# Kernel optimization log

Measured on AMD Instinct MI355X. Metric: run time of the kernel, lower is better.

Reference implementation:

```python
import jax, jax.numpy as jnp
import numpy as np

B, N, NFEAT, NHID, NHEADS, NCLASS, K1 = 4, 2048, 256, 64, 4, 32, 256
ALPHA = 0.2      # leaky relu slope
NEG = -9e15      # mask value used by the torch impl


def setup_inputs() -> dict:
    key = jax.random.key(0)
    ks = jax.random.split(key, 16)
    s = 0.05
    return {
        "x": jax.random.normal(ks[0], (B, N, NFEAT), jnp.float32),
        "adj": jax.random.randint(ks[1], (B, N, N), 0, 2).astype(jnp.int32),
        "one_hop_idcs": jax.random.randint(ks[2], (B, K1), 0, N),
        # multi-head GAT layer params (stacked over heads)
        "W": jax.random.normal(ks[3], (NHEADS, NFEAT, NHID), jnp.float32) * s,
        "a1": jax.random.normal(ks[4], (NHEADS, NHID), jnp.float32) * s,  # a[:nhid]
        "a2": jax.random.normal(ks[5], (NHEADS, NHID), jnp.float32) * s,  # a[nhid:]
        # output GAT layer params
        "Wo": jax.random.normal(ks[6], (NHEADS * NHID, NCLASS), jnp.float32) * s,
        "ao1": jax.random.normal(ks[7], (NCLASS,), jnp.float32) * s,
        "ao2": jax.random.normal(ks[8], (NCLASS,), jnp.float32) * s,
        # classifier: Linear(32, nclass) -> PReLU(nclass) -> Linear(nclass, 2)
        "W1": jax.random.normal(ks[9], (NCLASS, NCLASS), jnp.float32) * s,
        "b1": jnp.zeros((NCLASS,), jnp.float32),
        "prelu_w": jnp.full((NCLASS,), 0.25, jnp.float32),
        "W2": jax.random.normal(ks[10], (NCLASS, 2), jnp.float32) * s,
        "b2": jnp.zeros((2,), jnp.float32),
    }


def _gat_heads(x, W, a1, a2, adj):
    """Dense multi-head GAT. e_ij = leakyrelu(a^T [Wh_i || Wh_j]) computed
    as broadcast of two rank-1 projections (no [N,N,2d] concat tensor)."""
    Wh = jnp.einsum('bnf,hfd->bhnd', x, W)                 # [B,H,N,d]
    f1 = jnp.einsum('bhnd,hd->bhn', Wh, a1)                # src term
    f2 = jnp.einsum('bhnd,hd->bhn', Wh, a2)                # dst term
    e = jax.nn.leaky_relu(f1[:, :, :, None] + f2[:, :, None, :], ALPHA)
    e = jnp.where(adj[:, None, :, :] > 0, e, NEG)
    attn = jax.nn.softmax(e, axis=-1)                      # [B,H,N,N]
    h = jnp.einsum('bhnm,bhmd->bhnd', attn, Wh)            # [B,H,N,d]
    h = jax.nn.elu(h)                                      # concat=True -> elu
    # concat heads: [B,N,H*d]
    return h.transpose(0, 2, 1, 3).reshape(x.shape[0], x.shape[1], -1)


def _gat_out(x, Wo, ao1, ao2, adj):
    Wh = x @ Wo                                            # [B,N,nclass]
    f1 = Wh @ ao1
    f2 = Wh @ ao2
    e = jax.nn.leaky_relu(f1[:, :, None] + f2[:, None, :], ALPHA)
    e = jnp.where(adj > 0, e, NEG)
    attn = jax.nn.softmax(e, axis=-1)
    return attn @ Wh                                       # concat=False -> no elu here


def reference(x, adj, one_hop_idcs, W, a1, a2, Wo, ao1, ao2,
              W1, b1, prelu_w, W2, b2):
    h = _gat_heads(x, W, a1, a2, adj)          # [B,N,H*nhid]
    h = jax.nn.elu(_gat_out(h, Wo, ao1, ao2, adj))  # [B,N,nclass]
    # vectorized per-batch gather (replaces python loop over b)
    ef = jnp.take_along_axis(h, one_hop_idcs[:, :, None], axis=1)  # [B,K1,nclass]
    ef = ef.reshape(-1, h.shape[-1])
    y = ef @ W1 + b1
    y = jnp.where(y > 0, y, prelu_w * y)       # PReLU(nclass)
    return y @ W2 + b2                         # [B*K1, 2]
```

## Files before the change

kernel.cpp:

```cpp
#include <hip/hip_runtime.h>
#include <hip/hip_bf16.h>
#include <stdint.h>
#include <math.h>

#define BB 4
#define NN 2048
#define NFEAT 256
#define NHID 64
#define NHEADS 4
#define NCLASS 32
#define KK1 256
#define ALPHA 0.2f
#define LOG2E 1.4426950408889634f

typedef _Float16 f16x8 __attribute__((ext_vector_type(8)));
typedef _Float16 f16x4 __attribute__((ext_vector_type(4)));
typedef _Float16 h16x2 __attribute__((ext_vector_type(2)));
typedef float f32x4 __attribute__((ext_vector_type(4)));

__device__ __forceinline__ f16x8 ld8(const _Float16* p){
  f16x8 r;
  *(f16x4*)&r = *(const f16x4*)p;
  *((f16x4*)&r + 1) = *(const f16x4*)(p + 4);
  return r;
}

__device__ __forceinline__ h16x2 pk2(float a, float b){
  auto v = __builtin_amdgcn_cvt_pkrtz(a, b);
  h16x2 r;
  __builtin_memcpy(&r, &v, sizeof(r));
  return r;
}

__global__ void __launch_bounds__(256) pack_adj(const int* __restrict__ adj,
                                                unsigned long long* __restrict__ bits,
                                                int* __restrict__ cnt){
  __shared__ int csum[4];
  int row = blockIdx.x;
  const int* arow = adj + (size_t)row * NN;
  int lane = threadIdx.x & 63, wv = threadIdx.x >> 6;
  int c = 0;
  #pragma unroll
  for (int it=0; it<NN/256; ++it){
    int j = it*256 + threadIdx.x;
    unsigned long long m = __ballot(arow[j] > 0);
    if (lane==0){ bits[(size_t)row*(NN/64) + it*4 + wv] = m; c += __popcll(m); }
  }
  if (lane==0) csum[wv] = c;
  __syncthreads();
  if (threadIdx.x==0) cnt[row] = csum[0]+csum[1]+csum[2]+csum[3];
}

__global__ void __launch_bounds__(256) wh_proj2(const float* __restrict__ x,
        const float* __restrict__ W, const float* __restrict__ a1, const float* __restrict__ a2,
        _Float16* __restrict__ whT, float* __restrict__ f1l, float* __restrict__ f2l){
  __shared__ __align__(16) float xs[64*65];
  __shared__ float red1[4][64];
  __shared__ float red2[4][64];
  int bh = blockIdx.x >> 5;
  int i0 = (blockIdx.x & 31) * 64;
  int b = bh >> 2, h = bh & 3;
  int tid = threadIdx.x;
  int lane = tid & 63;
  int dbase = __builtin_amdgcn_readfirstlane(tid >> 6) * 16;
  float acc[16];
  #pragma unroll
  for (int dd=0; dd<16; ++dd) acc[dd] = 0.f;
  for (int kc=0; kc<4; ++kc){
    int kb = kc*64;
    __syncthreads();
    #pragma unroll
    for (int t=0; t<4; ++t){
      int row = t*16 + (tid>>4);
      int f4 = (tid&15)*4;
      float4 v = *(const float4*)(x + ((size_t)(b*NN + i0 + row))*NFEAT + kb + f4);
      xs[row*65 + f4 + 0] = v.x;
      xs[row*65 + f4 + 1] = v.y;
      xs[row*65 + f4 + 2] = v.z;
      xs[row*65 + f4 + 3] = v.w;
    }
    __syncthreads();
    const float* Wb = W + (size_t)h*NFEAT*NHID + (size_t)kb*NHID + dbase;
    #pragma unroll 4
    for (int f=0; f<64; ++f){
      float xv = xs[lane*65 + f];
      const float* wr = Wb + f*NHID;
      #pragma unroll
      for (int dd=0; dd<16; ++dd) acc[dd] = fmaf(xv, wr[dd], acc[dd]);
    }
  }
  float p1 = 0.f, p2 = 0.f;
  #pragma unroll
  for (int dd=0; dd<16; ++dd){
    int d = dbase + dd;
    whT[((size_t)bh*NHID + d)*NN + i0 + lane] = (_Float16)acc[dd];
    p1 = fmaf(acc[dd], a1[h*NHID + d], p1);
    p2 = fmaf(acc[dd], a2[h*NHID + d], p2);
  }
  int wv = tid >> 6;
  red1[wv][lane] = p1;
  red2[wv][lane] = p2;
  __syncthreads();
  if (tid < 64){
    float s1 = red1[0][tid]+red1[1][tid]+red1[2][tid]+red1[3][tid];
    float s2 = red2[0][tid]+red2[1][tid]+red2[2][tid]+red2[3][tid];
    f1l[(size_t)bh*NN + i0 + tid] = s1 * LOG2E;
    f2l[(size_t)bh*NN + i0 + tid] = s2 * LOG2E;
  }
}

__global__ void __launch_bounds__(256) attn_l1(
        const unsigned long long* __restrict__ bits,
        const _Float16* __restrict__ whT,
        const float* __restrict__ f1l, const float* __restrict__ f2l,
        const int* __restrict__ cnt_in,
        float* __restrict__ dst){
  const int JC = 128, PITCH = 132;
  __shared__ __align__(16) _Float16 whs[64*PITCH];
  __shared__ __align__(16) _Float16 wts[32*PITCH];
  __shared__ float ils[32];
  int tile = blockIdx.x & 63;
  int bh = blockIdx.x >> 6;
  int b = bh >> 2, h = bh & 3;
  int i0 = tile*32;
  int tid = threadIdx.x;
  int lane = tid & 63, wv = tid >> 6;
  int q = lane >> 4, col = lane & 15;
  int r = tid >> 3, jg = (tid & 7) * 16;
  float f1r = f1l[(size_t)bh*NN + i0 + r];
  bool czr = (cnt_in[b*NN + i0 + r] == 0);
  const unsigned short* mrow = (const unsigned short*)(bits + ((size_t)(b*NN + i0 + r))*(NN/64));
  const float* f2p = f2l + (size_t)bh*NN;
  const _Float16* whg = whT + (size_t)bh*NHID*NN;
  float lacc = 0.f;
  f32x4 c0 = {0.f,0.f,0.f,0.f}, c1 = {0.f,0.f,0.f,0.f};
  for (int it=0; it<NN/JC; ++it){
    __syncthreads();
    #pragma unroll
    for (int dd=0; dd<4; ++dd){
      int d = (tid>>4) + dd*16;
      int j8 = (tid&15)*8;
      uint4 v = *(const uint4*)(whg + (size_t)d*NN + it*JC + j8);
      uint2* w2 = (uint2*)&whs[d*PITCH + j8];
      w2[0] = uint2{v.x, v.y};
      w2[1] = uint2{v.z, v.w};
    }
    {
      unsigned int m16 = mrow[it*8 + (tid&7)];
      const float* fp = f2p + it*JC + jg;
      float4 fa = *(const float4*)(fp);
      float4 fb = *(const float4*)(fp+4);
      float4 fc = *(const float4*)(fp+8);
      float4 fd = *(const float4*)(fp+12);
      float fv[16] = {fa.x,fa.y,fa.z,fa.w, fb.x,fb.y,fb.z,fb.w,
                      fc.x,fc.y,fc.z,fc.w, fd.x,fd.y,fd.z,fd.w};
      h16x2 wp[8];
      #pragma unroll
      for (int p=0; p<8; ++p){
        float s0 = f1r + fv[2*p];
        float s1 = f1r + fv[2*p+1];
        s0 = (m16 & (1u<<(2*p)))   ? s0 : -1e5f;
        s1 = (m16 & (1u<<(2*p+1))) ? s1 : -1e5f;
        float e0 = fmaxf(s0, ALPHA*s0);
        float e1 = fmaxf(s1, ALPHA*s1);
        float w0 = exp2f(e0);
        float w1 = exp2f(e1);
        lacc += w0 + w1;
        wp[p] = pk2(w0, w1);
      }
      if (__builtin_expect(czr, 0)){
        h16x2 one2 = {(_Float16)1.f, (_Float16)1.f};
        #pragma unroll
        for (int p=0; p<8; ++p) wp[p] = one2;
      }
      uint2* wdst = (uint2*)&wts[r*PITCH + jg];
      const uint2* wsrc = (const uint2*)&wp[0];
      wdst[0]=wsrc[0]; wdst[1]=wsrc[1]; wdst[2]=wsrc[2]; wdst[3]=wsrc[3];
    }
    __syncthreads();
    #pragma unroll
    for (int ks=0; ks<4; ++ks){
      int kb = ks*32 + q*8;
      f16x8 a0 = ld8(&wts[col*PITCH + kb]);
      f16x8 a1v = ld8(&wts[(16+col)*PITCH + kb]);
      f16x8 bv = ld8(&whs[(wv*16+col)*PITCH + kb]);
      c0 = __builtin_amdgcn_mfma_f32_16x16x32_f16(a0, bv, c0, 0, 0, 0);
      c1 = __builtin_amdgcn_mfma_f32_16x16x32_f16(a1v, bv, c1, 0, 0, 0);
    }
  }
  lacc += __shfl_xor(lacc, 1, 64);
  lacc += __shfl_xor(lacc, 2, 64);
  lacc += __shfl_xor(lacc, 4, 64);
  if ((tid & 7) == 0) ils[r] = czr ? (1.0f/(float)NN) : 1.0f/lacc;
  __syncthreads();
  int dloc = wv*16 + col;
  #pragma unroll
  for (int mt=0; mt<2; ++mt){
    #pragma unroll
    for (int reg=0; reg<4; ++reg){
      int ir = mt*16 + q*4 + reg;
      float v = (mt==0 ? c0[reg] : c1[reg]) * ils[ir];
      v = v > 0.f ? v : expm1f(v);
      dst[((size_t)(b*NN + i0 + ir))*(NHEADS*NHID) + h*NHID + dloc] = v;
    }
  }
}

__global__ void __launch_bounds__(256) out_proj2(const float* __restrict__ h1,
        const float* __restrict__ Wo, const float* __restrict__ ao1, const float* __restrict__ ao2,
        _Float16* __restrict__ whT2, float* __restrict__ f1ol, float* __restrict__ f2ol){
  __shared__ __align__(16) float xs[64*65];
  __shared__ float red1[4][64];
  __shared__ float red2[4][64];
  int b = blockIdx.x >> 5;
  int i0 = (blockIdx.x & 31) * 64;
  int tid = threadIdx.x;
  int lane = tid & 63;
  int dbase = __builtin_amdgcn_readfirstlane(tid >> 6) * 8;
  float acc[8];
  #pragma unroll
  for (int dd=0; dd<8; ++dd) acc[dd] = 0.f;
  for (int kc=0; kc<4; ++kc){
    int kb = kc*64;
    __syncthreads();
    #pragma unroll
    for (int t=0; t<4; ++t){
      int row = t*16 + (tid>>4);
      int f4 = (tid&15)*4;
      float4 v = *(const float4*)(h1 + ((size_t)(b*NN + i0 + row))*256 + kb + f4);
      xs[row*65 + f4 + 0] = v.x;
      xs[row*65 + f4 + 1] = v.y;
      xs[row*65 + f4 + 2] = v.z;
      xs[row*65 + f4 + 3] = v.w;
    }
    __syncthreads();
    #pragma unroll 4
    for (int f=0; f<64; ++f){
      float xv = xs[lane*65 + f];
      const float* wr = Wo + (size_t)(kb+f)*NCLASS + dbase;
      #pragma unroll
      for (int dd=0; dd<8; ++dd) acc[dd] = fmaf(xv, wr[dd], acc[dd]);
    }
  }
  float p1 = 0.f, p2 = 0.f;
  #pragma unroll
  for (int dd=0; dd<8; ++dd){
    int d = dbase + dd;
    whT2[((size_t)b*NCLASS + d)*NN + i0 + lane] = (_Float16)acc[dd];
    p1 = fmaf(acc[dd], ao1[d], p1);
    p2 = fmaf(acc[dd], ao2[d], p2);
  }
  int wv = tid >> 6;
  red1[wv][lane] = p1;
  red2[wv][lane] = p2;
  __syncthreads();
  if (tid < 64){
    float s1 = red1[0][tid]+red1[1][tid]+red1[2][tid]+red1[3][tid];
    float s2 = red2[0][tid]+red2[1][tid]+red2[2][tid]+red2[3][tid];
    f1ol[(size_t)b*NN + i0 + tid] = s1 * LOG2E;
    f2ol[(size_t)b*NN + i0 + tid] = s2 * LOG2E;
  }
}

__global__ void __launch_bounds__(256) attn_l2(
        const unsigned long long* __restrict__ bits,
        const _Float16* __restrict__ whT2,
        const float* __restrict__ f1ol, const float* __restrict__ f2ol,
        const int* __restrict__ cnt_in, const int* __restrict__ oh,
        float* __restrict__ pc, float* __restrict__ pl){
  const int JC = 128, PITCH = 132;
  __shared__ __align__(16) _Float16 whs[32*PITCH];
  __shared__ __align__(16) _Float16 wts[32*PITCH];
  int blk = blockIdx.x;
  int js = blk & 7, kt = (blk>>3) & 7, b = blk >> 6;
  int tid = threadIdx.x;
  int lane = tid & 63, wv = tid >> 6;
  int q = lane >> 4, col = lane & 15;
  int r = tid >> 3, jg = (tid & 7) * 16;
  int row_i = oh[b*KK1 + kt*32 + r];
  float f1r = f1ol[b*NN + row_i];
  bool czr = (cnt_in[b*NN + row_i] == 0);
  const unsigned short* mrow = (const unsigned short*)(bits + ((size_t)(b*NN + row_i))*(NN/64));
  const float* f2p = f2ol + (size_t)b*NN;
  const _Float16* whg = whT2 + (size_t)b*NCLASS*NN;
  float lacc = 0.f;
  f32x4 c0 = {0.f,0.f,0.f,0.f};
  int mt = wv & 1, nt = wv >> 1;
  for (int ii=0; ii<2; ++ii){
    int it = js*2 + ii;
    __syncthreads();
    #pragma unroll
    for (int dd=0; dd<2; ++dd){
      int d = (tid>>4) + dd*16;
      int j8 = (tid&15)*8;
      uint4 v = *(const uint4*)(whg + (size_t)d*NN + it*JC + j8);
      uint2* w2 = (uint2*)&whs[d*PITCH + j8];
      w2[0] = uint2{v.x, v.y};
      w2[1] = uint2{v.z, v.w};
    }
    {
      unsigned int m16 = mrow[it*8 + (tid&7)];
      const float* fp = f2p + it*JC + jg;
      float4 fa = *(const float4*)(fp);
      float4 fb = *(const float4*)(fp+4);
      float4 fc = *(const float4*)(fp+8);
      float4 fd = *(const float4*)(fp+12);
      float fv[16] = {fa.x,fa.y,fa.z,fa.w, fb.x,fb.y,fb.z,fb.w,
                      fc.x,fc.y,fc.z,fc.w, fd.x,fd.y,fd.z,fd.w};
      h16x2 wp[8];
      #pragma unroll
      for (int p=0; p<8; ++p){
        float s0 = f1r + fv[2*p];
        float s1 = f1r + fv[2*p+1];
        s0 = (m16 & (1u<<(2*p)))   ? s0 : -1e5f;
        s1 = (m16 & (1u<<(2*p+1))) ? s1 : -1e5f;
        float e0 = fmaxf(s0, ALPHA*s0);
        float e1 = fmaxf(s1, ALPHA*s1);
        float w0 = exp2f(e0);
        float w1 = exp2f(e1);
        lacc += w0 + w1;
        wp[p] = pk2(w0, w1);
      }
      if (__builtin_expect(czr, 0)){
        h16x2 one2 = {(_Float16)1.f, (_Float16)1.f};
        #pragma unroll
        for (int p=0; p<8; ++p) wp[p] = one2;
        lacc += 16.f;
      }
      uint2* wdst = (uint2*)&wts[r*PITCH + jg];
      const uint2* wsrc = (const uint2*)&wp[0];
      wdst[0]=wsrc[0]; wdst[1]=wsrc[1]; wdst[2]=wsrc[2]; wdst[3]=wsrc[3];
    }
    __syncthreads();
    #pragma unroll
    for (int ks=0; ks<4; ++ks){
      int kb = ks*32 + q*8;
      f16x8 a0 = ld8(&wts[(mt*16+col)*PITCH + kb]);
      f16x8 bv = ld8(&whs[(nt*16+col)*PITCH + kb]);
      c0 = __builtin_amdgcn_mfma_f32_16x16x32_f16(a0, bv, c0, 0, 0, 0);
    }
  }
  lacc += __shfl_xor(lacc, 1, 64);
  lacc += __shfl_xor(lacc, 2, 64);
  lacc += __shfl_xor(lacc, 4, 64);
  if ((tid & 7) == 0) pl[blk*32 + r] = lacc;
  int dloc = nt*16 + col;
  #pragma unroll
  for (int reg=0; reg<4; ++reg){
    int ir = mt*16 + q*4 + reg;
    pc[(size_t)blk*1024 + ir*32 + dloc] = c0[reg];
  }
}

__global__ void __launch_bounds__(256) classify2(const float* __restrict__ pc,
        const float* __restrict__ pl,
        const float* __restrict__ W1, const float* __restrict__ b1,
        const float* __restrict__ pw, const float* __restrict__ W2, const float* __restrict__ b2,
        float* __restrict__ out){
  __shared__ float efs[4][32];
  int wv = threadIdx.x >> 6;
  int lane = threadIdx.x & 63;
  int row = blockIdx.x*4 + wv;
  int b = row >> 8, k = row & 255;
  int kt = k >> 5, r = k & 31;
  int base = (b*8 + kt)*8;
  if (lane < 32){
    float s = 0.f, l = 0.f;
    #pragma unroll
    for (int js=0; js<8; ++js){
      s += pc[(size_t)(base+js)*1024 + r*32 + lane];
      l += pl[(base+js)*32 + r];
    }
    float v = s / l;
    v = v > 0.f ? v : expm1f(v);
    efs[wv][lane] = v;
  }
  __syncthreads();
  const float* ef = efs[wv];
  int c = lane & 31;
  float y = b1[c];
  #pragma unroll 8
  for (int kk=0; kk<32; ++kk) y += ef[kk] * W1[kk*32 + c];
  y = y > 0.f ? y : pw[c]*y;
  float o0 = y * W2[c*2+0];
  float o1 = y * W2[c*2+1];
  #pragma unroll
  for (int o=16;o>0;o>>=1){ o0 += __shfl_xor(o0,o,64); o1 += __shfl_xor(o1,o,64); }
  if (lane==0){ out[row*2+0] = o0 + b2[0]; out[row*2+1] = o1 + b2[1]; }
}

extern "C" void kernel_launch(void* const* d_in, const int* in_sizes, int n_in,
                              void* d_out, int out_size, void* d_ws, size_t ws_size,
                              hipStream_t stream) {
  const float* x    = (const float*)d_in[0];
  const int*   adj  = (const int*)  d_in[1];
  const int*   oh   = (const int*)  d_in[2];
  const float* W    = (const float*)d_in[3];
  const float* a1   = (const float*)d_in[4];
  const float* a2   = (const float*)d_in[5];
  const float* Wo   = (const float*)d_in[6];
  const float* ao1  = (const float*)d_in[7];
  const float* ao2  = (const float*)d_in[8];
  const float* W1   = (const float*)d_in[9];
  const float* b1   = (const float*)d_in[10];
  const float* pw   = (const float*)d_in[11];
  const float* W2   = (const float*)d_in[12];
  const float* b2   = (const float*)d_in[13];
  float* out = (float*)d_out;

  char* base = (char*)d_ws;
  size_t off = 0;
  auto alloc = [&](size_t bytes)->char*{
    char* p = base + off;
    off = (off + bytes + 255) & ~(size_t)255;
    return p;
  };
  unsigned long long* adjbits = (unsigned long long*)alloc((size_t)BB*NN*(NN/64)*8);
  int*   cnt1 = (int*)  alloc((size_t)BB*NN*4);
  _Float16* WhT  = (_Float16*)alloc((size_t)BB*NHEADS*NHID*NN*2);
  float* f1l  = (float*)alloc((size_t)BB*NHEADS*NN*4);
  float* f2l  = (float*)alloc((size_t)BB*NHEADS*NN*4);
  float* h1   = (float*)alloc((size_t)BB*NN*(NHEADS*NHID)*4);
  _Float16* WhT2 = (_Float16*)alloc((size_t)BB*NCLASS*NN*2);
  float* f1ol = (float*)alloc((size_t)BB*NN*4);
  float* f2ol = (float*)alloc((size_t)BB*NN*4);
  float* pc   = (float*)alloc((size_t)256*1024*4);
  float* pl   = (float*)alloc((size_t)256*32*4);

  pack_adj<<<BB*NN, 256, 0, stream>>>(adj, adjbits, cnt1);
  wh_proj2<<<BB*NHEADS*(NN/64), 256, 0, stream>>>(x, W, a1, a2, WhT, f1l, f2l);
  attn_l1<<<BB*NHEADS*(NN/32), 256, 0, stream>>>(adjbits, WhT, f1l, f2l, cnt1, h1);
  out_proj2<<<BB*(NN/64), 256, 0, stream>>>(h1, Wo, ao1, ao2, WhT2, f1ol, f2ol);
  attn_l2<<<BB*8*8, 256, 0, stream>>>(adjbits, WhT2, f1ol, f2ol, cnt1, oh, pc, pl);
  classify2<<<(BB*KK1)/4, 256, 0, stream>>>(pc, pl, W1, b1, pw, W2, b2, out);
}
```

Baseline: 233.8 us.

## Double-buffer attn_l1 LDS tiles with register prefetch and branchless masking

```diff
diff --git a/kernel.cpp b/kernel.cpp
--- a/kernel.cpp
+++ b/kernel.cpp
@@ -30,6 +30,14 @@
   h16x2 r;
   __builtin_memcpy(&r, &v, sizeof(r));
   return r;
+}
+
+__device__ __forceinline__ float fexp2(float x){
+#if __has_builtin(__builtin_amdgcn_exp2f)
+  return __builtin_amdgcn_exp2f(x);
+#else
+  return exp2f(x);
+#endif
 }
 
 __global__ void __launch_bounds__(256) pack_adj(const int* __restrict__ adj,
@@ -115,9 +123,9 @@
         const float* __restrict__ f1l, const float* __restrict__ f2l,
         const int* __restrict__ cnt_in,
         float* __restrict__ dst){
-  const int JC = 128, PITCH = 132;
-  __shared__ __align__(16) _Float16 whs[64*PITCH];
-  __shared__ __align__(16) _Float16 wts[32*PITCH];
+  const int JC = 128, PITCH = 136;
+  __shared__ __align__(16) _Float16 whs[2][64*PITCH];
+  __shared__ __align__(16) _Float16 wts[2][32*PITCH];
   __shared__ float ils[32];
   int tile = blockIdx.x & 63;
   int bh = blockIdx.x >> 6;
@@ -130,63 +138,79 @@
   float f1r = f1l[(size_t)bh*NN + i0 + r];
   bool czr = (cnt_in[b*NN + i0 + r] == 0);
   const unsigned short* mrow = (const unsigned short*)(bits + ((size_t)(b*NN + i0 + r))*(NN/64));
-  const float* f2p = f2l + (size_t)bh*NN;
+  const float* f2p = f2l + (size_t)bh*NN + jg;
   const _Float16* whg = whT + (size_t)bh*NHID*NN;
+  const _Float16* wsrc = whg + (size_t)(tid>>4)*NN + (tid&15)*8;
   float lacc = 0.f;
   f32x4 c0 = {0.f,0.f,0.f,0.f}, c1 = {0.f,0.f,0.f,0.f};
-  for (int it=0; it<NN/JC; ++it){
-    __syncthreads();
-    #pragma unroll
-    for (int dd=0; dd<4; ++dd){
-      int d = (tid>>4) + dd*16;
-      int j8 = (tid&15)*8;
-      uint4 v = *(const uint4*)(whg + (size_t)d*NN + it*JC + j8);
-      uint2* w2 = (uint2*)&whs[d*PITCH + j8];
-      w2[0] = uint2{v.x, v.y};
-      w2[1] = uint2{v.z, v.w};
-    }
-    {
-      unsigned int m16 = mrow[it*8 + (tid&7)];
-      const float* fp = f2p + it*JC + jg;
-      float4 fa = *(const float4*)(fp);
-      float4 fb = *(const float4*)(fp+4);
-      float4 fc = *(const float4*)(fp+8);
-      float4 fd = *(const float4*)(fp+12);
-      float fv[16] = {fa.x,fa.y,fa.z,fa.w, fb.x,fb.y,fb.z,fb.w,
-                      fc.x,fc.y,fc.z,fc.w, fd.x,fd.y,fd.z,fd.w};
-      h16x2 wp[8];
+  uint4 vr0, vr1, vr2, vr3;
+  float4 fa, fb, fc, fd;
+  unsigned int m16 = 0;
+
+  auto issue_loads = [&](int it){
+    const _Float16* ws = wsrc + it*JC;
+    vr0 = *(const uint4*)(ws);
+    vr1 = *(const uint4*)(ws + 16*NN);
+    vr2 = *(const uint4*)(ws + 32*NN);
+    vr3 = *(const uint4*)(ws + 48*NN);
+    const float* fp = f2p + it*JC;
+    fa = *(const float4*)(fp);
+    fb = *(const float4*)(fp+4);
+    fc = *(const float4*)(fp+8);
+    fd = *(const float4*)(fp+12);
+    m16 = mrow[it*8 + (tid&7)];
+  };
+
+  auto stage = [&](int nb){
+    _Float16* wb = &whs[nb][(tid>>4)*PITCH + (tid&15)*8];
+    *(uint4*)(wb)             = vr0;
+    *(uint4*)(wb + 16*PITCH)  = vr1;
+    *(uint4*)(wb + 32*PITCH)  = vr2;
+    *(uint4*)(wb + 48*PITCH)  = vr3;
+    float fv[16] = {fa.x,fa.y,fa.z,fa.w, fb.x,fb.y,fb.z,fb.w,
+                    fc.x,fc.y,fc.z,fc.w, fd.x,fd.y,fd.z,fd.w};
+    h16x2 wp[8];
+    #pragma unroll
+    for (int p=0; p<8; ++p){
+      float s0 = f1r + fv[2*p];
+      float s1 = f1r + fv[2*p+1];
+      float w0 = fexp2(fmaxf(s0, ALPHA*s0));
+      float w1 = fexp2(fmaxf(s1, ALPHA*s1));
+      unsigned mb0 = (unsigned)(((int)(m16 << (31 - 2*p))) >> 31);
+      unsigned mb1 = (unsigned)(((int)(m16 << (30 - 2*p))) >> 31);
+      w0 = __uint_as_float(__float_as_uint(w0) & mb0);
+      w1 = __uint_as_float(__float_as_uint(w1) & mb1);
+      lacc += w0 + w1;
+      wp[p] = pk2(w0, w1);
+    }
+    if (__builtin_expect(czr, 0)){
+      h16x2 one2 = {(_Float16)1.f, (_Float16)1.f};
       #pragma unroll
-      for (int p=0; p<8; ++p){
-        float s0 = f1r + fv[2*p];
-        float s1 = f1r + fv[2*p+1];
-        s0 = (m16 & (1u<<(2*p)))   ? s0 : -1e5f;
-        s1 = (m16 & (1u<<(2*p+1))) ? s1 : -1e5f;
-        float e0 = fmaxf(s0, ALPHA*s0);
-        float e1 = fmaxf(s1, ALPHA*s1);
-        float w0 = exp2f(e0);
-        float w1 = exp2f(e1);
-        lacc += w0 + w1;
-        wp[p] = pk2(w0, w1);
-      }
-      if (__builtin_expect(czr, 0)){
-        h16x2 one2 = {(_Float16)1.f, (_Float16)1.f};
-        #pragma unroll
-        for (int p=0; p<8; ++p) wp[p] = one2;
-      }
-      uint2* wdst = (uint2*)&wts[r*PITCH + jg];
-      const uint2* wsrc = (const uint2*)&wp[0];
-      wdst[0]=wsrc[0]; wdst[1]=wsrc[1]; wdst[2]=wsrc[2]; wdst[3]=wsrc[3];
-    }
-    __syncthreads();
+      for (int p=0; p<8; ++p) wp[p] = one2;
+    }
+    uint4* wdst = (uint4*)&wts[nb][r*PITCH + jg];
+    wdst[0] = *(const uint4*)&wp[0];
+    wdst[1] = *(const uint4*)&wp[4];
+  };
+
+  issue_loads(0);
+  stage(0);
+  __syncthreads();
+  #pragma unroll 2
+  for (int it=0; it<16; ++it){
+    int cur = it & 1;
+    if (it < 15) issue_loads(it+1);
     #pragma unroll
     for (int ks=0; ks<4; ++ks){
       int kb = ks*32 + q*8;
-      f16x8 a0 = ld8(&wts[col*PITCH + kb]);
-      f16x8 a1v = ld8(&wts[(16+col)*PITCH + kb]);
-      f16x8 bv = ld8(&whs[(wv*16+col)*PITCH + kb]);
+      f16x8 a0  = *(const f16x8*)&wts[cur][col*PITCH + kb];
+      f16x8 a1v = *(const f16x8*)&wts[cur][(16+col)*PITCH + kb];
+      f16x8 bv  = *(const f16x8*)&whs[cur][(wv*16+col)*PITCH + kb];
       c0 = __builtin_amdgcn_mfma_f32_16x16x32_f16(a0, bv, c0, 0, 0, 0);
       c1 = __builtin_amdgcn_mfma_f32_16x16x32_f16(a1v, bv, c1, 0, 0, 0);
     }
+    if (it < 15) stage(cur ^ 1);
+    __syncthreads();
   }
   lacc += __shfl_xor(lacc, 1, 64);
   lacc += __shfl_xor(lacc, 2, 64);
```

Result: faster. 217.9 us (-6.8%).

## Split layer-1 attention over key halves and combine partials in a new kernel

Applied to the files above, without the earlier changes.

```diff
diff --git a/kernel.cpp b/kernel.cpp
--- a/kernel.cpp
+++ b/kernel.cpp
@@ -30,6 +30,14 @@
   h16x2 r;
   __builtin_memcpy(&r, &v, sizeof(r));
   return r;
+}
+
+__device__ __forceinline__ float fexp2(float x){
+#if __has_builtin(__builtin_amdgcn_exp2f)
+  return __builtin_amdgcn_exp2f(x);
+#else
+  return exp2f(x);
+#endif
 }
 
 __global__ void __launch_bounds__(256) pack_adj(const int* __restrict__ adj,
@@ -114,13 +122,14 @@
         const _Float16* __restrict__ whT,
         const float* __restrict__ f1l, const float* __restrict__ f2l,
         const int* __restrict__ cnt_in,
-        float* __restrict__ dst){
+        float* __restrict__ pc, float* __restrict__ pl){
   const int JC = 128, PITCH = 132;
   __shared__ __align__(16) _Float16 whs[64*PITCH];
   __shared__ __align__(16) _Float16 wts[32*PITCH];
-  __shared__ float ils[32];
-  int tile = blockIdx.x & 63;
-  int bh = blockIdx.x >> 6;
+  int blk = blockIdx.x;
+  int js = blk & 1;
+  int tile = (blk >> 1) & 63;
+  int bh = blk >> 7;
   int b = bh >> 2, h = bh & 3;
   int i0 = tile*32;
   int tid = threadIdx.x;
@@ -134,7 +143,8 @@
   const _Float16* whg = whT + (size_t)bh*NHID*NN;
   float lacc = 0.f;
   f32x4 c0 = {0.f,0.f,0.f,0.f}, c1 = {0.f,0.f,0.f,0.f};
-  for (int it=0; it<NN/JC; ++it){
+  for (int ii=0; ii<8; ++ii){
+    int it = js*8 + ii;
     __syncthreads();
     #pragma unroll
     for (int dd=0; dd<4; ++dd){
@@ -159,12 +169,12 @@
       for (int p=0; p<8; ++p){
         float s0 = f1r + fv[2*p];
         float s1 = f1r + fv[2*p+1];
-        s0 = (m16 & (1u<<(2*p)))   ? s0 : -1e5f;
-        s1 = (m16 & (1u<<(2*p+1))) ? s1 : -1e5f;
-        float e0 = fmaxf(s0, ALPHA*s0);
-        float e1 = fmaxf(s1, ALPHA*s1);
-        float w0 = exp2f(e0);
-        float w1 = exp2f(e1);
+        float w0 = fexp2(fmaxf(s0, ALPHA*s0));
+        float w1 = fexp2(fmaxf(s1, ALPHA*s1));
+        unsigned mb0 = (unsigned)(((int)(m16 << (31 - 2*p))) >> 31);
+        unsigned mb1 = (unsigned)(((int)(m16 << (30 - 2*p))) >> 31);
+        w0 = __uint_as_float(__float_as_uint(w0) & mb0);
+        w1 = __uint_as_float(__float_as_uint(w1) & mb1);
         lacc += w0 + w1;
         wp[p] = pk2(w0, w1);
       }
@@ -191,19 +201,47 @@
   lacc += __shfl_xor(lacc, 1, 64);
   lacc += __shfl_xor(lacc, 2, 64);
   lacc += __shfl_xor(lacc, 4, 64);
-  if ((tid & 7) == 0) ils[r] = czr ? (1.0f/(float)NN) : 1.0f/lacc;
-  __syncthreads();
+  float* plh = pl + (size_t)js*BB*NHEADS*NN;
+  if ((tid & 7) == 0) plh[(size_t)bh*NN + i0 + r] = czr ? (float)(NN/2) : lacc;
+  float* pch = pc + (size_t)js*BB*NN*(NHEADS*NHID);
   int dloc = wv*16 + col;
   #pragma unroll
   for (int mt=0; mt<2; ++mt){
     #pragma unroll
     for (int reg=0; reg<4; ++reg){
       int ir = mt*16 + q*4 + reg;
-      float v = (mt==0 ? c0[reg] : c1[reg]) * ils[ir];
-      v = v > 0.f ? v : expm1f(v);
-      dst[((size_t)(b*NN + i0 + ir))*(NHEADS*NHID) + h*NHID + dloc] = v;
-    }
-  }
+      pch[((size_t)(b*NN + i0 + ir))*(NHEADS*NHID) + h*NHID + dloc] =
+          (mt==0 ? c0[reg] : c1[reg]);
+    }
+  }
+}
+
+__global__ void __launch_bounds__(256) combine_h1(const float* __restrict__ pc,
+        const float* __restrict__ pl, float* __restrict__ h1){
+  const float* pa = pc;
+  const float* pb = pc + (size_t)BB*NN*(NHEADS*NHID);
+  const float* la = pl;
+  const float* lb = pl + (size_t)BB*NHEADS*NN;
+  int row = blockIdx.x*8 + (threadIdx.x>>5);
+  int c = (threadIdx.x & 31) * 8;
+  int b = row >> 11, i = row & (NN-1);
+  int h = c >> 6;
+  size_t idx = (size_t)row*(NHEADS*NHID) + c;
+  float l = la[((size_t)(b*NHEADS + h))*NN + i] + lb[((size_t)(b*NHEADS + h))*NN + i];
+  float il = 1.f / l;
+  float4 a0 = *(const float4*)(pa + idx);
+  float4 a1 = *(const float4*)(pa + idx + 4);
+  float4 b0 = *(const float4*)(pb + idx);
+  float4 b1 = *(const float4*)(pb + idx + 4);
+  float v[8] = {a0.x+b0.x, a0.y+b0.y, a0.z+b0.z, a0.w+b0.w,
+                a1.x+b1.x, a1.y+b1.y, a1.z+b1.z, a1.w+b1.w};
+  #pragma unroll
+  for (int k=0; k<8; ++k){
+    float t = v[k] * il;
+    v[k] = t > 0.f ? t : expm1f(t);
+  }
+  *(float4*)(h1 + idx)     = float4{v[0],v[1],v[2],v[3]};
+  *(float4*)(h1 + idx + 4) = float4{v[4],v[5],v[6],v[7]};
 }
 
 __global__ void __launch_bounds__(256) out_proj2(const float* __restrict__ h1,
@@ -421,6 +459,8 @@
   float* f1l  = (float*)alloc((size_t)BB*NHEADS*NN*4);
   float* f2l  = (float*)alloc((size_t)BB*NHEADS*NN*4);
   float* h1   = (float*)alloc((size_t)BB*NN*(NHEADS*NHID)*4);
+  float* pc1  = (float*)alloc((size_t)2*BB*NN*(NHEADS*NHID)*4);
+  float* pl1  = (float*)alloc((size_t)2*BB*NHEADS*NN*4);
   _Float16* WhT2 = (_Float16*)alloc((size_t)BB*NCLASS*NN*2);
   float* f1ol = (float*)alloc((size_t)BB*NN*4);
   float* f2ol = (float*)alloc((size_t)BB*NN*4);
@@ -429,7 +469,8 @@
 
   pack_adj<<<BB*NN, 256, 0, stream>>>(adj, adjbits, cnt1);
   wh_proj2<<<BB*NHEADS*(NN/64), 256, 0, stream>>>(x, W, a1, a2, WhT, f1l, f2l);
-  attn_l1<<<BB*NHEADS*(NN/32), 256, 0, stream>>>(adjbits, WhT, f1l, f2l, cnt1, h1);
+  attn_l1<<<BB*NHEADS*(NN/32)*2, 256, 0, stream>>>(adjbits, WhT, f1l, f2l, cnt1, pc1, pl1);
+  combine_h1<<<(BB*NN)/8, 256, 0, stream>>>(pc1, pl1, h1);
   out_proj2<<<BB*(NN/64), 256, 0, stream>>>(h1, Wo, ao1, ao2, WhT2, f1ol, f2ol);
   attn_l2<<<BB*8*8, 256, 0, stream>>>(adjbits, WhT2, f1ol, f2ol, cnt1, oh, pc, pl);
   classify2<<<(BB*KK1)/4, 256, 0, stream>>>(pc, pl, W1, b1, pw, W2, b2, out);
```

Result: no change. 237.6 us (+1.6%).
